# Kernel tuning notes

Measured on AMD Instinct MI355X. Metric: run time of the kernel, lower is better.

The kernel has to match this reference:

```python
import math
import jax, jax.numpy as jnp
import numpy as np

B, S, D_MODEL = 4, 2048, 1024
N_HEADS, D_KV = 16, 64
INNER = N_HEADS * D_KV
NUM_BUCKETS = 32
MAX_DISTANCE = 128


def _relative_position_bucket(relative_position, bidirectional=True,
                              num_buckets=32, max_distance=128):
    # Faithful port of T5Attention._relative_position_bucket
    ret = jnp.zeros_like(relative_position)
    n = -relative_position
    if bidirectional:
        num_buckets //= 2
        ret = ret + (n < 0).astype(jnp.int32) * num_buckets
        n = jnp.abs(n)
    else:
        n = jnp.maximum(n, 0)
    max_exact = num_buckets // 2
    is_small = n < max_exact
    # safe log: n>=max_exact wherever this branch is selected
    val_if_large = max_exact + (
        jnp.log(jnp.maximum(n, 1).astype(jnp.float32) / max_exact)
        / math.log(max_distance / max_exact) * (num_buckets - max_exact)
    ).astype(jnp.int32)
    val_if_large = jnp.minimum(val_if_large, num_buckets - 1)
    return ret + jnp.where(is_small, n, val_if_large)


def setup_inputs() -> dict:
    key = jax.random.key(0)
    k_h, k_q, k_k, k_v, k_o, k_e = jax.random.split(key, 6)
    std = D_MODEL ** -0.5
    return {
        "hidden_states": jax.random.normal(k_h, (B, S, D_MODEL), dtype=jnp.float32),
        "Wq": jax.random.normal(k_q, (D_MODEL, INNER), dtype=jnp.float32) * std,
        "Wk": jax.random.normal(k_k, (D_MODEL, INNER), dtype=jnp.float32) * std,
        "Wv": jax.random.normal(k_v, (D_MODEL, INNER), dtype=jnp.float32) * std,
        "Wo": jax.random.normal(k_o, (INNER, D_MODEL), dtype=jnp.float32) * std,
        "rel_emb": jax.random.normal(k_e, (NUM_BUCKETS, N_HEADS), dtype=jnp.float32) * std,
    }


def reference(hidden_states, Wq, Wk, Wv, Wo, rel_emb):
    b, s, _ = hidden_states.shape
    # QKV projections (T5: no bias, no 1/sqrt(d) scaling of scores)
    def shape_heads(x):  # [b, s, inner] -> [b, h, s, d_kv]
        return x.reshape(b, s, N_HEADS, D_KV).transpose(0, 2, 1, 3)
    q = shape_heads(hidden_states @ Wq)
    k = shape_heads(hidden_states @ Wk)
    v = shape_heads(hidden_states @ Wv)

    scores = jnp.einsum("bhqd,bhkd->bhqk", q, k)  # [b, h, s, s]

    # relative position bias: sequential_relative_position + bucket + embed
    context_pos = jnp.arange(s, dtype=jnp.int32)[:, None]
    memory_pos = jnp.arange(s, dtype=jnp.int32)[None, :]
    rel_pos = memory_pos - context_pos  # [s, s]
    rp_bucket = _relative_position_bucket(rel_pos, bidirectional=True,
                                          num_buckets=NUM_BUCKETS,
                                          max_distance=MAX_DISTANCE)
    bias = rel_emb[rp_bucket]                       # [s, s, h]
    bias = bias.transpose(2, 0, 1)[None]            # [1, h, s, s]

    weights = jax.nn.softmax(scores + bias, axis=-1)
    context = jnp.einsum("bhqk,bhkd->bhqd", weights, v)
    context = context.transpose(0, 2, 1, 3).reshape(b, s, INNER)
    return context @ Wo
```

## Files before the change

kernel.cpp:

```cpp
#include <hip/hip_runtime.h>

typedef __bf16 bf16_t;
typedef __bf16 bf16x4 __attribute__((ext_vector_type(4)));
typedef __bf16 bf16x8 __attribute__((ext_vector_type(8)));
typedef float f32x4 __attribute__((ext_vector_type(4)));

#define NB 4
#define SS 2048
#define DM 1024
#define NH 16
#define DK 64
#define MM (NB*SS)
#define LOG2E 1.44269504f

__global__ __launch_bounds__(256) void k_prep(
    const float* __restrict__ H, bf16_t* __restrict__ Hbf,
    const float* __restrict__ W0, const float* __restrict__ W1,
    const float* __restrict__ W2, const float* __restrict__ W3,
    bf16_t* __restrict__ T0, bf16_t* __restrict__ T1,
    bf16_t* __restrict__ T2, bf16_t* __restrict__ T3,
    const float* __restrict__ rel_emb, float* __restrict__ biasT) {
  __shared__ float t[64][65];
  const int blk = blockIdx.x, tid = threadIdx.x;
  if (blk < 8192) {
    int i = blk * 256 + tid;
    float4 v = ((const float4*)H)[i];
    bf16x4 o = {(bf16_t)v.x, (bf16_t)v.y, (bf16_t)v.z, (bf16_t)v.w};
    *(bf16x4*)(Hbf + 4 * (size_t)i) = o;
  } else if (blk < 9216) {
    int tt = blk - 8192;
    int which = tt >> 8, rem = tt & 255;
    int k0 = (rem >> 4) * 64, n0 = (rem & 15) * 64;
    const float* W = which == 0 ? W0 : which == 1 ? W1 : which == 2 ? W2 : W3;
    bf16_t* T = which == 0 ? T0 : which == 1 ? T1 : which == 2 ? T2 : T3;
#pragma unroll
    for (int i = 0; i < 16; i++) {
      int idx = tid + i * 256; int r = idx >> 6, c = idx & 63;
      t[r][c] = W[(size_t)(k0 + r) * DM + n0 + c];
    }
    __syncthreads();
#pragma unroll
    for (int i = 0; i < 16; i++) {
      int idx = tid + i * 256; int r = idx >> 6, c = idx & 63;
      T[(size_t)(n0 + r) * DM + k0 + c] = (bf16_t)t[c][r];
    }
  } else {
    int tt = (blk - 9216) * 256 + tid;
    if (tt < 2 * SS - 1) {
      int rel = tt - (SS - 1);
      int n = -rel;
      int ret = 0;
      if (n < 0) { ret = 16; n = -n; }
      int bucket;
      if (n < 8) bucket = n;
      else {
        int v = 8 + (int)(logf((float)n * 0.125f) * (8.0f / logf(16.0f)));
        bucket = v < 15 ? v : 15;
      }
      bucket += ret;
#pragma unroll
      for (int h = 0; h < NH; h++)
        biasT[h * (2 * SS - 1) + tt] = rel_emb[bucket * NH + h] * LOG2E;
    }
  }
}

__device__ __forceinline__ void gld16(const bf16_t* g, bf16_t* l) {
  __builtin_amdgcn_global_load_lds(
      (const __attribute__((address_space(1))) unsigned int*)g,
      (__attribute__((address_space(3))) unsigned int*)l, 16, 0, 0);
}

__device__ __forceinline__ void gemm_tile(const bf16_t* __restrict__ A,
                                          const bf16_t* __restrict__ Bt, const int K,
                                          const int m0, const int n0,
                                          bf16_t* As, bf16_t* Bs, f32x4 (&acc)[4][4]) {
  const int tid = threadIdx.x;
  const int lane = tid & 63, wave = tid >> 6;
  const int l15 = lane & 15, quad = lane >> 4;
  const int wm = (wave >> 1) * 64, wn = (wave & 1) * 64;
  const int wwu = __builtin_amdgcn_readfirstlane(wave);
  const f32x4 z4 = {0.f, 0.f, 0.f, 0.f};
#pragma unroll
  for (int i = 0; i < 4; i++)
#pragma unroll
    for (int j = 0; j < 4; j++) acc[i][j] = z4;

  const int rr = lane >> 2;
  const int cc = (lane & 3) * 8;
  for (int k0 = 0; k0 < K; k0 += 32) {
    __syncthreads();
    gld16(A + (size_t)(m0 + wwu * 32 + rr) * K + k0 + cc,       As + wwu * 1024);
    gld16(A + (size_t)(m0 + wwu * 32 + 16 + rr) * K + k0 + cc,  As + wwu * 1024 + 512);
    gld16(Bt + (size_t)(n0 + wwu * 32 + rr) * K + k0 + cc,      Bs + wwu * 1024);
    gld16(Bt + (size_t)(n0 + wwu * 32 + 16 + rr) * K + k0 + cc, Bs + wwu * 1024 + 512);
    __syncthreads();
    bf16x8 af[4], bfr[4];
#pragma unroll
    for (int i = 0; i < 4; i++) {
      af[i]  = *(const bf16x8*)(As + (wm + i * 16 + l15) * 32 + quad * 8);
      bfr[i] = *(const bf16x8*)(Bs + (wn + i * 16 + l15) * 32 + quad * 8);
    }
#pragma unroll
    for (int i = 0; i < 4; i++)
#pragma unroll
      for (int j = 0; j < 4; j++)
        acc[i][j] = __builtin_amdgcn_mfma_f32_16x16x32_bf16(af[i], bfr[j], acc[i][j], 0, 0, 0);
  }
}

__global__ __launch_bounds__(256) void k_gemm_qkv(
    const bf16_t* __restrict__ A, const bf16_t* __restrict__ Wqt,
    const bf16_t* __restrict__ Wkt, const bf16_t* __restrict__ Wvt,
    bf16_t* __restrict__ Q, bf16_t* __restrict__ Kf, bf16_t* __restrict__ Vf) {
  __shared__ bf16_t As[128 * 32];
  __shared__ bf16_t Bs[128 * 32];
  const int which = blockIdx.z;
  const bf16_t* Bt = which == 0 ? Wqt : (which == 1 ? Wkt : Wvt);
  const int m0 = blockIdx.x * 128, n0 = blockIdx.y * 128;
  f32x4 acc[4][4];
  gemm_tile(A, Bt, DM, m0, n0, As, Bs, acc);

  const int tid = threadIdx.x;
  const int lane = tid & 63, wave = tid >> 6;
  const int l15 = lane & 15, quad = lane >> 4;
  const int wm = (wave >> 1) * 64, wn = (wave & 1) * 64;

  if (which == 0) {
#pragma unroll
    for (int i = 0; i < 4; i++)
#pragma unroll
      for (int j = 0; j < 4; j++)
#pragma unroll
        for (int r = 0; r < 4; r++) {
          int m = m0 + wm + i * 16 + quad * 4 + r;
          int n = n0 + wn + j * 16 + l15;
          int b = m >> 11, s = m & (SS - 1);
          int h = n >> 6, d = n & 63;
          Q[(((size_t)(b * NH + h)) * SS + s) * DK + d] = (bf16_t)(acc[i][j][r] * LOG2E);
        }
  } else if (which == 1) {
#pragma unroll
    for (int i = 0; i < 4; i++)
#pragma unroll
      for (int j = 0; j < 4; j++)
#pragma unroll
        for (int r = 0; r < 4; r++) {
          int m = m0 + wm + i * 16 + quad * 4 + r;
          int n = n0 + wn + j * 16 + l15;
          int b = m >> 11, s = m & (SS - 1);
          int h = n >> 6, d = n & 63;
          int slot = 4 * ((s >> 5) & 1) + 2 * ((s >> 2) & 1) + (d >> 5);
          int fl = ((d >> 3) & 3) * 16 + 4 * ((s >> 3) & 3) + (s & 3);
          Kf[(((size_t)(b * NH + h) * 32 + (s >> 6)) * 8 + slot) * 512 + fl * 8 + (d & 7)] =
              (bf16_t)acc[i][j][r];
        }
  } else {
#pragma unroll
    for (int i = 0; i < 4; i++)
#pragma unroll
      for (int j = 0; j < 4; j++) {
        int m = m0 + wm + i * 16 + quad * 4;
        int n = n0 + wn + j * 16 + l15;
        int b = m >> 11, s = m & (SS - 1);
        int h = n >> 6, d = n & 63;
        int slot = 4 * ((s >> 5) & 1) + (d >> 4);
        int fl = ((s >> 3) & 3) * 16 + (d & 15);
        bf16x4 pk = {(bf16_t)acc[i][j][0], (bf16_t)acc[i][j][1],
                     (bf16_t)acc[i][j][2], (bf16_t)acc[i][j][3]};
        *(bf16x4*)(&Vf[(((size_t)(b * NH + h) * 32 + (s >> 6)) * 8 + slot) * 512 +
                       fl * 8 + (s & 7)]) = pk;
      }
  }
}

__global__ __launch_bounds__(256, 2) void k_attn(const bf16_t* __restrict__ Qg,
                                                 const bf16_t* __restrict__ Kf,
                                                 const bf16_t* __restrict__ Vf,
                                                 const float* __restrict__ biasT,
                                                 bf16_t* __restrict__ ctx) {
  const int bh = blockIdx.y;
  const int b = bh >> 4, h = bh & 15;
  const int it0 = blockIdx.x * 128;
  const bf16_t* Qp = Qg + ((size_t)bh * SS + it0) * DK;
  const float* biasH = biasT + h * (2 * SS - 1);

  __shared__ float bias2[512][2];
  __shared__ float OsumS[2][4][16];
  __shared__ f32x4 Ored[2 * 4 * 4 * 64];

  const int tid = threadIdx.x;
  const int lane = tid & 63, wave = tid >> 6;
  const int l15 = lane & 15, quad = lane >> 4;
  const int kh = wave & 1, qh = wave >> 1;

  for (int w = tid; w < 512; w += 256) {
    int g = w - 256 + (SS - 1);
    bias2[w][0] = biasH[g];
    bias2[w][1] = biasH[g + 1];
  }
  const float Bpos = biasH[(SS - 1) + 1024];
  const float Bneg = biasH[(SS - 1) - 1024];

  const bf16_t* KfB = Kf + (size_t)bh * 32 * 4096 + lane * 8;
  const bf16_t* VfB = Vf + (size_t)bh * 32 * 4096 + lane * 8;
  auto loadfrag = [&](int it, bf16x8 (&kf)[2][2], bf16x8 (&vf)[4]) {
    const bf16_t* kb = KfB + (size_t)it * 4096;
#pragma unroll
    for (int t = 0; t < 2; t++)
#pragma unroll
      for (int hf = 0; hf < 2; hf++)
        kf[t][hf] = *(const bf16x8*)(kb + ((2 * kh + t) * 2 + hf) * 512);
    const bf16_t* vb = VfB + (size_t)it * 4096;
#pragma unroll
    for (int ni = 0; ni < 4; ni++)
      vf[ni] = *(const bf16x8*)(vb + (kh * 4 + ni) * 512);
  };

  bf16x8 qf[4][2];
#pragma unroll
  for (int mi = 0; mi < 4; mi++) {
    const bf16_t* qr = Qp + (size_t)(64 * qh + mi * 16 + l15) * DK + quad * 8;
    qf[mi][0] = *(const bf16x8*)qr;
    qf[mi][1] = *(const bf16x8*)(qr + 32);
  }

  f32x4 accO[4][4], accS[4];
  const f32x4 z4 = {0.f, 0.f, 0.f, 0.f};
#pragma unroll
  for (int mi = 0; mi < 4; mi++) {
    accS[mi] = z4;
#pragma unroll
    for (int ni = 0; ni < 4; ni++) accO[mi][ni] = z4;
  }
  const bf16_t one = (bf16_t)1.0f;
  const bf16x8 ones = {one, one, one, one, one, one, one, one};

  const int wb0 = 32 * kh + 8 * quad - 64 * qh - l15 - it0 + 256;

  auto body = [&](int it, bf16x8 (&kf)[2][2], bf16x8 (&vf)[4]) {
    const int diff = it * 64 - it0;
    const bool band = (diff >= -128) && (diff < 256);
    const float cconst = diff >= 256 ? Bpos : Bneg;
    const f32x4 csplat = {cconst, cconst, cconst, cconst};
    const int jb = it * 64 + wb0;
#pragma unroll
    for (int mi = 0; mi < 4; mi++) {
      f32x4 c0, c1;
      if (band) {
        const int w = jb - mi * 16;
        float2 a0 = *(const float2*)bias2[w],     b0 = *(const float2*)bias2[w + 2];
        float2 a1 = *(const float2*)bias2[w + 4], b1 = *(const float2*)bias2[w + 6];
        c0 = f32x4{a0.x, a0.y, b0.x, b0.y};
        c1 = f32x4{a1.x, a1.y, b1.x, b1.y};
      } else {
        c0 = csplat;
        c1 = csplat;
      }
      f32x4 s0 = __builtin_amdgcn_mfma_f32_16x16x32_bf16(
          kf[0][1], qf[mi][1],
          __builtin_amdgcn_mfma_f32_16x16x32_bf16(kf[0][0], qf[mi][0], c0, 0, 0, 0), 0, 0, 0);
      f32x4 s1 = __builtin_amdgcn_mfma_f32_16x16x32_bf16(
          kf[1][1], qf[mi][1],
          __builtin_amdgcn_mfma_f32_16x16x32_bf16(kf[1][0], qf[mi][0], c1, 0, 0, 0), 0, 0, 0);
      bf16x8 pf = {(bf16_t)__builtin_amdgcn_exp2f(s0[0]), (bf16_t)__builtin_amdgcn_exp2f(s0[1]),
                   (bf16_t)__builtin_amdgcn_exp2f(s0[2]), (bf16_t)__builtin_amdgcn_exp2f(s0[3]),
                   (bf16_t)__builtin_amdgcn_exp2f(s1[0]), (bf16_t)__builtin_amdgcn_exp2f(s1[1]),
                   (bf16_t)__builtin_amdgcn_exp2f(s1[2]), (bf16_t)__builtin_amdgcn_exp2f(s1[3])};
#pragma unroll
      for (int ni = 0; ni < 4; ni++)
        accO[mi][ni] = __builtin_amdgcn_mfma_f32_16x16x32_bf16(vf[ni], pf, accO[mi][ni], 0, 0, 0);
      accS[mi] = __builtin_amdgcn_mfma_f32_16x16x32_bf16(ones, pf, accS[mi], 0, 0, 0);
    }
  };

  bf16x8 kfA[2][2], vfA[4], kfB[2][2], vfB[4];
  loadfrag(0, kfA, vfA);
  __syncthreads();

  for (int it = 0; it < 32; it += 2) {
    loadfrag(it + 1, kfB, vfB);
    body(it, kfA, vfA);
    if (it + 2 < 32) loadfrag(it + 2, kfA, vfA);
    body(it + 1, kfB, vfB);
  }

  __syncthreads();
  if (kh) {
#pragma unroll
    for (int mi = 0; mi < 4; mi++) {
#pragma unroll
      for (int ni = 0; ni < 4; ni++)
        Ored[((qh * 4 + mi) * 4 + ni) * 64 + lane] = accO[mi][ni];
      if (quad == 0) OsumS[qh][mi][l15] = accS[mi][0];
    }
  }
  __syncthreads();
  if (!kh) {
#pragma unroll
    for (int mi = 0; mi < 4; mi++) {
      float l = accS[mi][0] + OsumS[qh][mi][l15];
      float inv = 1.0f / l;
      int srow = it0 + 64 * qh + mi * 16 + l15;
#pragma unroll
      for (int ni = 0; ni < 4; ni++) {
        f32x4 o = accO[mi][ni] + Ored[((qh * 4 + mi) * 4 + ni) * 64 + lane];
        bf16x4 pk = {(bf16_t)(o[0] * inv), (bf16_t)(o[1] * inv),
                     (bf16_t)(o[2] * inv), (bf16_t)(o[3] * inv)};
        *(bf16x4*)(&ctx[((size_t)(b * SS + srow)) * DM + h * DK + ni * 16 + quad * 4]) = pk;
      }
    }
  }
}

__global__ __launch_bounds__(256) void k_gemm_out(const bf16_t* __restrict__ A,
                                                  const bf16_t* __restrict__ Wot,
                                                  float* __restrict__ out) {
  __shared__ bf16_t As[128 * 32];
  __shared__ bf16_t Bs[128 * 32];
  const int m0 = blockIdx.x * 128, n0 = blockIdx.y * 128;
  f32x4 acc[4][4];
  gemm_tile(A, Wot, DM, m0, n0, As, Bs, acc);

  const int tid = threadIdx.x;
  const int lane = tid & 63, wave = tid >> 6;
  const int l15 = lane & 15, quad = lane >> 4;
  const int wm = (wave >> 1) * 64, wn = (wave & 1) * 64;
#pragma unroll
  for (int i = 0; i < 4; i++)
#pragma unroll
    for (int j = 0; j < 4; j++)
#pragma unroll
      for (int r = 0; r < 4; r++) {
        int m = m0 + wm + i * 16 + quad * 4 + r;
        int n = n0 + wn + j * 16 + l15;
        out[(size_t)m * DM + n] = acc[i][j][r];
      }
}

extern "C" void kernel_launch(void* const* d_in, const int* in_sizes, int n_in,
                              void* d_out, int out_size, void* d_ws, size_t ws_size,
                              hipStream_t stream) {
  (void)in_sizes; (void)n_in; (void)out_size; (void)ws_size;
  const float* H  = (const float*)d_in[0];
  const float* Wq = (const float*)d_in[1];
  const float* Wk = (const float*)d_in[2];
  const float* Wv = (const float*)d_in[3];
  const float* Wo = (const float*)d_in[4];
  const float* rel = (const float*)d_in[5];
  float* out = (float*)d_out;

  char* w = (char*)d_ws;
  bf16_t* Hbf = (bf16_t*)w; w += (size_t)MM * DM * 2;
  bf16_t* Wqt = (bf16_t*)w; w += (size_t)DM * DM * 2;
  bf16_t* Wkt = (bf16_t*)w; w += (size_t)DM * DM * 2;
  bf16_t* Wvt = (bf16_t*)w; w += (size_t)DM * DM * 2;
  bf16_t* Wot = (bf16_t*)w; w += (size_t)DM * DM * 2;
  bf16_t* Q   = (bf16_t*)w; w += (size_t)MM * DM * 2;
  bf16_t* Kf  = (bf16_t*)w; w += (size_t)MM * DM * 2;
  bf16_t* Vf  = (bf16_t*)w; w += (size_t)MM * DM * 2;
  bf16_t* CTX = (bf16_t*)w; w += (size_t)MM * DM * 2;
  float* biasT = (float*)w;

  k_prep<<<9232, 256, 0, stream>>>(H, Hbf, Wq, Wk, Wv, Wo, Wqt, Wkt, Wvt, Wot, rel, biasT);
  k_gemm_qkv<<<dim3(MM / 128, DM / 128, 3), 256, 0, stream>>>(Hbf, Wqt, Wkt, Wvt, Q, Kf, Vf);
  k_attn<<<dim3(SS / 128, NB * NH), 256, 0, stream>>>(Q, Kf, Vf, biasT, CTX);
  k_gemm_out<<<dim3(MM / 128, DM / 128), 256, 0, stream>>>(CTX, Wot, out);
}
```

Baseline: 267.0 us.

## Stage K/V tiles in LDS and split attention waves by query rows

The attention kernel now stages each 64-key K/V tile into double-buffered shared memory with gld16 loads, so all four waves share one copy instead of each reading its own fragments from global memory. Each wave owns 32 query rows over the full key range, which removes the cross-wave reduction of partial outputs and row sums at the end. Block indices are also remapped across heads, likely to spread work across XCDs and caches, and the occupancy hint rises to three blocks per CU. The cost is a __syncthreads per key tile and more LDS traffic per iteration.

```diff
diff --git a/kernel.cpp b/kernel.cpp
--- a/kernel.cpp
+++ b/kernel.cpp
@@ -174,25 +174,27 @@
   }
 }
 
-__global__ __launch_bounds__(256, 2) void k_attn(const bf16_t* __restrict__ Qg,
+__global__ __launch_bounds__(256, 3) void k_attn(const bf16_t* __restrict__ Qg,
                                                  const bf16_t* __restrict__ Kf,
                                                  const bf16_t* __restrict__ Vf,
                                                  const float* __restrict__ biasT,
                                                  bf16_t* __restrict__ ctx) {
-  const int bh = blockIdx.y;
+  const int lin = blockIdx.x + 16 * blockIdx.y;
+  const int nid = (lin & 7) * 128 + (lin >> 3);
+  const int bh = nid >> 4;
+  const int it0 = (nid & 15) * 128;
   const int b = bh >> 4, h = bh & 15;
-  const int it0 = blockIdx.x * 128;
   const bf16_t* Qp = Qg + ((size_t)bh * SS + it0) * DK;
   const float* biasH = biasT + h * (2 * SS - 1);
 
   __shared__ float bias2[512][2];
-  __shared__ float OsumS[2][4][16];
-  __shared__ f32x4 Ored[2 * 4 * 4 * 64];
+  __shared__ bf16_t lK[2][4096];
+  __shared__ bf16_t lV[2][4096];
 
   const int tid = threadIdx.x;
   const int lane = tid & 63, wave = tid >> 6;
   const int l15 = lane & 15, quad = lane >> 4;
-  const int kh = wave & 1, qh = wave >> 1;
+  const int wvu = __builtin_amdgcn_readfirstlane(wave);
 
   for (int w = tid; w < 512; w += 256) {
     int g = w - 256 + (SS - 1);
@@ -202,33 +204,30 @@
   const float Bpos = biasH[(SS - 1) + 1024];
   const float Bneg = biasH[(SS - 1) - 1024];
 
-  const bf16_t* KfB = Kf + (size_t)bh * 32 * 4096 + lane * 8;
-  const bf16_t* VfB = Vf + (size_t)bh * 32 * 4096 + lane * 8;
-  auto loadfrag = [&](int it, bf16x8 (&kf)[2][2], bf16x8 (&vf)[4]) {
-    const bf16_t* kb = KfB + (size_t)it * 4096;
-#pragma unroll
-    for (int t = 0; t < 2; t++)
-#pragma unroll
-      for (int hf = 0; hf < 2; hf++)
-        kf[t][hf] = *(const bf16x8*)(kb + ((2 * kh + t) * 2 + hf) * 512);
-    const bf16_t* vb = VfB + (size_t)it * 4096;
-#pragma unroll
-    for (int ni = 0; ni < 4; ni++)
-      vf[ni] = *(const bf16x8*)(vb + (kh * 4 + ni) * 512);
+  const bf16_t* KfB = Kf + (size_t)bh * 32 * 4096;
+  const bf16_t* VfB = Vf + (size_t)bh * 32 * 4096;
+  const int so = wvu * 1024 + lane * 8;
+  auto stage = [&](int it, int bufi) {
+    const bf16_t* kg = KfB + (size_t)it * 4096 + so;
+    const bf16_t* vg = VfB + (size_t)it * 4096 + so;
+    gld16(kg,       lK[bufi] + wvu * 1024);
+    gld16(kg + 512, lK[bufi] + wvu * 1024 + 512);
+    gld16(vg,       lV[bufi] + wvu * 1024);
+    gld16(vg + 512, lV[bufi] + wvu * 1024 + 512);
   };
 
-  bf16x8 qf[4][2];
-#pragma unroll
-  for (int mi = 0; mi < 4; mi++) {
-    const bf16_t* qr = Qp + (size_t)(64 * qh + mi * 16 + l15) * DK + quad * 8;
+  bf16x8 qf[2][2];
+#pragma unroll
+  for (int mi = 0; mi < 2; mi++) {
+    const bf16_t* qr = Qp + (size_t)(32 * wave + mi * 16 + l15) * DK + quad * 8;
     qf[mi][0] = *(const bf16x8*)qr;
     qf[mi][1] = *(const bf16x8*)(qr + 32);
   }
 
-  f32x4 accO[4][4], accS[4];
+  f32x4 accO[2][4], accS[2];
   const f32x4 z4 = {0.f, 0.f, 0.f, 0.f};
 #pragma unroll
-  for (int mi = 0; mi < 4; mi++) {
+  for (int mi = 0; mi < 2; mi++) {
     accS[mi] = z4;
 #pragma unroll
     for (int ni = 0; ni < 4; ni++) accO[mi][ni] = z4;
@@ -236,79 +235,75 @@
   const bf16_t one = (bf16_t)1.0f;
   const bf16x8 ones = {one, one, one, one, one, one, one, one};
 
-  const int wb0 = 32 * kh + 8 * quad - 64 * qh - l15 - it0 + 256;
-
-  auto body = [&](int it, bf16x8 (&kf)[2][2], bf16x8 (&vf)[4]) {
+  const int wb0 = 8 * quad - 32 * wave - l15 - it0 + 256;
+
+  stage(0, 0);
+
+  for (int it = 0; it < 32; ++it) {
+    const int buf = it & 1;
+    __syncthreads();
+    if (it + 1 < 32) stage(it + 1, buf ^ 1);
+
     const int diff = it * 64 - it0;
     const bool band = (diff >= -128) && (diff < 256);
     const float cconst = diff >= 256 ? Bpos : Bneg;
     const f32x4 csplat = {cconst, cconst, cconst, cconst};
-    const int jb = it * 64 + wb0;
-#pragma unroll
-    for (int mi = 0; mi < 4; mi++) {
-      f32x4 c0, c1;
-      if (band) {
-        const int w = jb - mi * 16;
-        float2 a0 = *(const float2*)bias2[w],     b0 = *(const float2*)bias2[w + 2];
-        float2 a1 = *(const float2*)bias2[w + 4], b1 = *(const float2*)bias2[w + 6];
-        c0 = f32x4{a0.x, a0.y, b0.x, b0.y};
-        c1 = f32x4{a1.x, a1.y, b1.x, b1.y};
-      } else {
-        c0 = csplat;
-        c1 = csplat;
+
+    bf16x8 kfr[4][2], vfr[8];
+#pragma unroll
+    for (int kt = 0; kt < 4; kt++)
+#pragma unroll
+      for (int hf = 0; hf < 2; hf++)
+        kfr[kt][hf] = *(const bf16x8*)(lK[buf] + (kt * 2 + hf) * 512 + lane * 8);
+#pragma unroll
+    for (int sl = 0; sl < 8; sl++)
+      vfr[sl] = *(const bf16x8*)(lV[buf] + sl * 512 + lane * 8);
+
+#pragma unroll
+    for (int mi = 0; mi < 2; mi++)
+#pragma unroll
+      for (int k2 = 0; k2 < 2; k2++) {
+        f32x4 c0, c1;
+        if (band) {
+          const int w = it * 64 + 32 * k2 + wb0 - mi * 16;
+          float2 a0 = *(const float2*)bias2[w],     b0 = *(const float2*)bias2[w + 2];
+          float2 a1 = *(const float2*)bias2[w + 4], b1 = *(const float2*)bias2[w + 6];
+          c0 = f32x4{a0.x, a0.y, b0.x, b0.y};
+          c1 = f32x4{a1.x, a1.y, b1.x, b1.y};
+        } else {
+          c0 = csplat;
+          c1 = csplat;
+        }
+        f32x4 s0 = __builtin_amdgcn_mfma_f32_16x16x32_bf16(
+            kfr[2 * k2][1], qf[mi][1],
+            __builtin_amdgcn_mfma_f32_16x16x32_bf16(kfr[2 * k2][0], qf[mi][0], c0, 0, 0, 0),
+            0, 0, 0);
+        f32x4 s1 = __builtin_amdgcn_mfma_f32_16x16x32_bf16(
+            kfr[2 * k2 + 1][1], qf[mi][1],
+            __builtin_amdgcn_mfma_f32_16x16x32_bf16(kfr[2 * k2 + 1][0], qf[mi][0], c1, 0, 0, 0),
+            0, 0, 0);
+        bf16x8 pf = {(bf16_t)__builtin_amdgcn_exp2f(s0[0]), (bf16_t)__builtin_amdgcn_exp2f(s0[1]),
+                     (bf16_t)__builtin_amdgcn_exp2f(s0[2]), (bf16_t)__builtin_amdgcn_exp2f(s0[3]),
+                     (bf16_t)__builtin_amdgcn_exp2f(s1[0]), (bf16_t)__builtin_amdgcn_exp2f(s1[1]),
+                     (bf16_t)__builtin_amdgcn_exp2f(s1[2]), (bf16_t)__builtin_amdgcn_exp2f(s1[3])};
+#pragma unroll
+        for (int ni = 0; ni < 4; ni++)
+          accO[mi][ni] = __builtin_amdgcn_mfma_f32_16x16x32_bf16(vfr[k2 * 4 + ni], pf,
+                                                                 accO[mi][ni], 0, 0, 0);
+        accS[mi] = __builtin_amdgcn_mfma_f32_16x16x32_bf16(ones, pf, accS[mi], 0, 0, 0);
       }
-      f32x4 s0 = __builtin_amdgcn_mfma_f32_16x16x32_bf16(
-          kf[0][1], qf[mi][1],
-          __builtin_amdgcn_mfma_f32_16x16x32_bf16(kf[0][0], qf[mi][0], c0, 0, 0, 0), 0, 0, 0);
-      f32x4 s1 = __builtin_amdgcn_mfma_f32_16x16x32_bf16(
-          kf[1][1], qf[mi][1],
-          __builtin_amdgcn_mfma_f32_16x16x32_bf16(kf[1][0], qf[mi][0], c1, 0, 0, 0), 0, 0, 0);
-      bf16x8 pf = {(bf16_t)__builtin_amdgcn_exp2f(s0[0]), (bf16_t)__builtin_amdgcn_exp2f(s0[1]),
-                   (bf16_t)__builtin_amdgcn_exp2f(s0[2]), (bf16_t)__builtin_amdgcn_exp2f(s0[3]),
-                   (bf16_t)__builtin_amdgcn_exp2f(s1[0]), (bf16_t)__builtin_amdgcn_exp2f(s1[1]),
-                   (bf16_t)__builtin_amdgcn_exp2f(s1[2]), (bf16_t)__builtin_amdgcn_exp2f(s1[3])};
-#pragma unroll
-      for (int ni = 0; ni < 4; ni++)
-        accO[mi][ni] = __builtin_amdgcn_mfma_f32_16x16x32_bf16(vf[ni], pf, accO[mi][ni], 0, 0, 0);
-      accS[mi] = __builtin_amdgcn_mfma_f32_16x16x32_bf16(ones, pf, accS[mi], 0, 0, 0);
-    }
-  };
-
-  bf16x8 kfA[2][2], vfA[4], kfB[2][2], vfB[4];
-  loadfrag(0, kfA, vfA);
-  __syncthreads();
-
-  for (int it = 0; it < 32; it += 2) {
-    loadfrag(it + 1, kfB, vfB);
-    body(it, kfA, vfA);
-    if (it + 2 < 32) loadfrag(it + 2, kfA, vfA);
-    body(it + 1, kfB, vfB);
-  }
-
-  __syncthreads();
-  if (kh) {
-#pragma unroll
-    for (int mi = 0; mi < 4; mi++) {
-#pragma unroll
-      for (int ni = 0; ni < 4; ni++)
-        Ored[((qh * 4 + mi) * 4 + ni) * 64 + lane] = accO[mi][ni];
-      if (quad == 0) OsumS[qh][mi][l15] = accS[mi][0];
-    }
-  }
-  __syncthreads();
-  if (!kh) {
-#pragma unroll
-    for (int mi = 0; mi < 4; mi++) {
-      float l = accS[mi][0] + OsumS[qh][mi][l15];
-      float inv = 1.0f / l;
-      int srow = it0 + 64 * qh + mi * 16 + l15;
-#pragma unroll
-      for (int ni = 0; ni < 4; ni++) {
-        f32x4 o = accO[mi][ni] + Ored[((qh * 4 + mi) * 4 + ni) * 64 + lane];
-        bf16x4 pk = {(bf16_t)(o[0] * inv), (bf16_t)(o[1] * inv),
-                     (bf16_t)(o[2] * inv), (bf16_t)(o[3] * inv)};
-        *(bf16x4*)(&ctx[((size_t)(b * SS + srow)) * DM + h * DK + ni * 16 + quad * 4]) = pk;
-      }
+  }
+
+#pragma unroll
+  for (int mi = 0; mi < 2; mi++) {
+    float inv = 1.0f / accS[mi][0];
+    int srow = it0 + 32 * wave + mi * 16 + l15;
+#pragma unroll
+    for (int ni = 0; ni < 4; ni++) {
+      f32x4 o = accO[mi][ni];
+      bf16x4 pk = {(bf16_t)(o[0] * inv), (bf16_t)(o[1] * inv),
+                   (bf16_t)(o[2] * inv), (bf16_t)(o[3] * inv)};
+      *(bf16x4*)(&ctx[((size_t)(b * SS + srow)) * DM + h * DK + ni * 16 + quad * 4]) = pk;
     }
   }
 }
```

After: 267.1 us. No clear change (+0.0%).
